# Kernel optimization log

Measured on AMD Instinct MI355X. Metric: run time of the kernel, lower is better.

The kernel has to match this reference:

```python
import jax, jax.numpy as jnp
import numpy as np

R = 64      # residual_channels
S = 128     # skip_channels
N_BLOCKS = 3
N_LAYERS = 10
L = N_BLOCKS * N_LAYERS  # 30 dilated blocks total


def _causal_conv_k2(x, W, b, dilation):
    """Causal dilated conv1d with kernel_size=2.
    x: [B, Cin, T], W: [Cout, Cin, 2], b: [Cout].
    out[t] = W[:,:,0] @ x[t - dilation] + W[:,:,1] @ x[t] + b  (zero-padded).
    """
    x_prev = jnp.pad(x, ((0, 0), (0, 0), (dilation, 0)))[:, :, :-dilation]
    return (jnp.einsum('oc,bct->bot', W[:, :, 0], x_prev)
            + jnp.einsum('oc,bct->bot', W[:, :, 1], x)
            + b[None, :, None])


def _conv1x1(x, W, b):
    # W: [Cout, Cin, 1]
    return jnp.einsum('oc,bct->bot', W[:, :, 0], x) + b[None, :, None]


def setup_inputs() -> dict:
    key = jax.random.key(0)
    ks = jax.random.split(key, 16)
    sc = 0.1
    inp = {
        'x': jax.random.normal(ks[0], (4, 1, 16384), dtype=jnp.float32),
        'w_causal': jax.random.normal(ks[1], (R, 1, 2), dtype=jnp.float32) * sc,
        'b_causal': jnp.zeros((R,), dtype=jnp.float32),
        'Wf': jax.random.normal(ks[2], (L, R, R, 2), dtype=jnp.float32) * sc,
        'bf': jnp.zeros((L, R), dtype=jnp.float32),
        'Wg': jax.random.normal(ks[3], (L, R, R, 2), dtype=jnp.float32) * sc,
        'bg': jnp.zeros((L, R), dtype=jnp.float32),
        'Wr': jax.random.normal(ks[4], (L, R, R, 1), dtype=jnp.float32) * sc,
        'br': jnp.zeros((L, R), dtype=jnp.float32),
        'Ws': jax.random.normal(ks[5], (L, S, R, 1), dtype=jnp.float32) * sc,
        'bs': jnp.zeros((L, S), dtype=jnp.float32),
        'w_post': jax.random.normal(ks[6], (S, S, 1), dtype=jnp.float32) * sc,
        'b_post': jnp.zeros((S,), dtype=jnp.float32),
        'w_o1': jax.random.normal(ks[7], (S, S, 1), dtype=jnp.float32) * sc,
        'b_o1': jnp.zeros((S,), dtype=jnp.float32),
        'w_o2': jax.random.normal(ks[8], (1, S, 1), dtype=jnp.float32) * sc,
        'b_o2': jnp.zeros((1,), dtype=jnp.float32),
    }
    return inp


def reference(x, w_causal, b_causal, Wf, bf, Wg, bg, Wr, br, Ws, bs,
              w_post, b_post, w_o1, b_o1, w_o2, b_o2):
    # initial causal conv (kernel 2, dilation 1): [B,1,T] -> [B,R,T]
    h = _causal_conv_k2(x, w_causal, b_causal, 1)
    skip_sum = jnp.zeros((h.shape[0], S, h.shape[2]), dtype=h.dtype)
    for i in range(L):
        d = 2 ** (i % N_LAYERS)
        f = jnp.tanh(_causal_conv_k2(h, Wf[i], bf[i], d))
        g = jax.nn.sigmoid(_causal_conv_k2(h, Wg[i], bg[i], d))
        out = f * g
        h = _conv1x1(out, Wr[i], br[i]) + h
        skip_sum = skip_sum + _conv1x1(out, Ws[i], bs[i])
    s = jax.nn.relu(_conv1x1(skip_sum, w_post, b_post))
    s = jax.nn.relu(_conv1x1(s, w_o1, b_o1))
    return _conv1x1(s, w_o2, b_o2)  # [B, 1, T]
```

## Files before the change

kernel.cpp:

```cpp
#include <hip/hip_runtime.h>

#define RCH 64
#define SCH 128
#define NLAYERS 30
#define TLEN 16384
#define NB 4
#define LSTR 72

typedef _Float16 f16;
typedef _Float16 f16x8 __attribute__((ext_vector_type(8)));
typedef float f32x4 __attribute__((ext_vector_type(4)));

__global__ __launch_bounds__(256) void pack_all(
    const float* __restrict__ Wf, const float* __restrict__ Wg,
    const float* __restrict__ Wr, const float* __restrict__ Ws,
    const float* __restrict__ w_post, const float* __restrict__ w_o1,
    f16* __restrict__ wfgp, f16* __restrict__ wrsp,
    f16* __restrict__ wpostp, f16* __restrict__ wo1pp)
{
    int id = blockIdx.x * 256 + threadIdx.x;
    const int N1 = NLAYERS * 8 * 4 * 64;
    const int N2 = NLAYERS * 12 * 2 * 64;
    const int N3 = 8 * 4 * 64;
    union { f16 h8[8]; uint4 u; } pk;
    if (id < N1) {
        int l = id & 63, kt = (id >> 6) & 3, mt = (id >> 8) & 7, i = id >> 11;
        int m = mt * 16 + (l & 15);
        int kb = kt * 32 + (l >> 4) * 8;
        #pragma unroll
        for (int j = 0; j < 8; ++j) {
            int k = kb + j, tap = k >> 6, c = k & 63;
            float v = (m < 64) ? Wf[(((i * 64 + m) * 64 + c) << 1) + tap]
                               : Wg[(((i * 64 + m - 64) * 64 + c) << 1) + tap];
            pk.h8[j] = (f16)v;
        }
        *(uint4*)&wfgp[(size_t)id * 8] = pk.u;
    } else if (id < N1 + N2) {
        int id2 = id - N1;
        int l = id2 & 63, kt = (id2 >> 6) & 1, mt = (id2 >> 7) % 12, i = id2 / 1536;
        int m = mt * 16 + (l & 15);
        int cb = kt * 32 + (l >> 4) * 8;
        #pragma unroll
        for (int j = 0; j < 8; ++j) {
            int c = cb + j;
            float v = (m < 64) ? Wr[(i * 64 + m) * 64 + c]
                               : Ws[(i * 128 + m - 64) * 64 + c];
            pk.h8[j] = (f16)v;
        }
        *(uint4*)&wrsp[(size_t)id2 * 8] = pk.u;
    } else if (id < N1 + N2 + 2 * N3) {
        int id3 = id - N1 - N2;
        const float* src = (id3 < N3) ? w_post : w_o1;
        f16* dst = (id3 < N3) ? wpostp : wo1pp;
        int id4 = id3 & (N3 - 1);
        int l = id4 & 63, kt = (id4 >> 6) & 3, mt = (id4 >> 8) & 7;
        int m = mt * 16 + (l & 15);
        int cb = kt * 32 + (l >> 4) * 8;
        #pragma unroll
        for (int j = 0; j < 8; ++j)
            pk.h8[j] = (f16)src[m * 128 + cb + j];
        *(uint4*)&dst[(size_t)id4 * 8] = pk.u;
    }
}

__global__ __launch_bounds__(256) void init_f16(
    const float* __restrict__ x, const float* __restrict__ wc,
    const float* __restrict__ bc, f16* __restrict__ h)
{
    int id = blockIdx.x * 256 + threadIdx.x;
    int t = id & (TLEN - 1);
    float xc = x[id];
    float xp = (t > 0) ? x[id - 1] : 0.f;
    f16* dst = h + (size_t)id * 64;
    #pragma unroll
    for (int c0 = 0; c0 < 64; c0 += 8) {
        union { f16 h8[8]; uint4 u; } pk;
        #pragma unroll
        for (int j = 0; j < 8; ++j) {
            int c = c0 + j;
            pk.h8[j] = (f16)fmaf(wc[2 * c], xp, fmaf(wc[2 * c + 1], xc, bc[c]));
        }
        *(uint4*)&dst[c0] = pk.u;
    }
}

__global__ __launch_bounds__(256, 4) void layer_mfma(
    const f16* __restrict__ hin, f16* __restrict__ hout, f16* __restrict__ skipw,
    const f16* __restrict__ wfgp, const f16* __restrict__ wrsp,
    const float* __restrict__ bf, const float* __restrict__ bg,
    const float* __restrict__ br, const float* __restrict__ bs,
    int layer, int dil, int first)
{
    __shared__ f16 hcurT[64 * LSTR];
    __shared__ f16 hprvT[64 * LSTR];
    __shared__ f16 outT [64 * LSTR];
    int tid = threadIdx.x, lane = tid & 63, wv = tid >> 6;
    int kg = lane >> 4, ln = lane & 15;
    int bx = blockIdx.x, b = bx >> 8, t0 = (bx & 255) * 64;
    const f16* hb = hin + (size_t)b * TLEN * 64;

    {
        int row = tid >> 2, q = tid & 3;
        const f16* src = hb + (size_t)(t0 + row) * 64;
        *(uint4*)&hcurT[row * LSTR + q * 8]       = *(const uint4*)&src[q * 8];
        *(uint4*)&hcurT[row * LSTR + (q + 4) * 8] = *(const uint4*)&src[(q + 4) * 8];
        int tp = t0 + row - dil;
        if (tp >= 0) {
            const f16* sp = hb + (size_t)tp * 64;
            *(uint4*)&hprvT[row * LSTR + q * 8]       = *(const uint4*)&sp[q * 8];
            *(uint4*)&hprvT[row * LSTR + (q + 4) * 8] = *(const uint4*)&sp[(q + 4) * 8];
        } else {
            uint4 z = make_uint4(0, 0, 0, 0);
            *(uint4*)&hprvT[row * LSTR + q * 8]       = z;
            *(uint4*)&hprvT[row * LSTR + (q + 4) * 8] = z;
        }
    }
    __syncthreads();

    const f16* wl = wfgp + (size_t)layer * 32 * 64 * 8;
    f16x8 a0[4], a1[4];
    #pragma unroll
    for (int kt = 0; kt < 4; ++kt) {
        a0[kt] = *(const f16x8*)&wl[(size_t)((wv * 4 + kt) * 64 + lane) * 8];
        a1[kt] = *(const f16x8*)&wl[(size_t)(((wv + 4) * 4 + kt) * 64 + lane) * 8];
    }
    f32x4 af[4], ag[4];
    {
        float4 bvf = *(const float4*)(bf + layer * 64 + wv * 16 + kg * 4);
        float4 bvg = *(const float4*)(bg + layer * 64 + wv * 16 + kg * 4);
        #pragma unroll
        for (int ts = 0; ts < 4; ++ts) {
            af[ts] = (f32x4){bvf.x, bvf.y, bvf.z, bvf.w};
            ag[ts] = (f32x4){bvg.x, bvg.y, bvg.z, bvg.w};
        }
    }
    #pragma unroll
    for (int ts = 0; ts < 4; ++ts) {
        #pragma unroll
        for (int kt = 0; kt < 4; ++kt) {
            const f16* tile = (kt < 2) ? hprvT : hcurT;
            f16x8 bb = *(const f16x8*)&tile[(ts * 16 + ln) * LSTR + (kt & 1) * 32 + kg * 8];
            af[ts] = __builtin_amdgcn_mfma_f32_16x16x32_f16(a0[kt], bb, af[ts], 0, 0, 0);
            ag[ts] = __builtin_amdgcn_mfma_f32_16x16x32_f16(a1[kt], bb, ag[ts], 0, 0, 0);
        }
    }

    #pragma unroll
    for (int ts = 0; ts < 4; ++ts) {
        union { f16 h[4]; uint2 u; } pk;
        #pragma unroll
        for (int r = 0; r < 4; ++r) {
            float fv = af[ts][r], gv = ag[ts][r];
            float e2 = __expf(2.f * fv);
            float th = 1.f - 2.f * __builtin_amdgcn_rcpf(e2 + 1.f);
            float sg = __builtin_amdgcn_rcpf(1.f + __expf(-gv));
            pk.h[r] = (f16)(th * sg);
        }
        *(uint2*)&outT[(ts * 16 + ln) * LSTR + wv * 16 + kg * 4] = pk.u;
    }
    __syncthreads();

    const f16* wl2 = wrsp + (size_t)layer * 24 * 64 * 8;
    int mt0 = wv * 3;
    f16x8 a2[3][2];
    #pragma unroll
    for (int m = 0; m < 3; ++m)
        #pragma unroll
        for (int kt = 0; kt < 2; ++kt)
            a2[m][kt] = *(const f16x8*)&wl2[(size_t)(((mt0 + m) * 2 + kt) * 64 + lane) * 8];
    f32x4 ac[3][4];
    #pragma unroll
    for (int m = 0; m < 3; ++m) {
        int mtt = mt0 + m;
        const float* bp = (mtt < 4) ? (br + layer * 64 + mtt * 16 + kg * 4)
                                    : (bs + layer * 128 + (mtt - 4) * 16 + kg * 4);
        float4 bv = *(const float4*)bp;
        #pragma unroll
        for (int ts = 0; ts < 4; ++ts)
            ac[m][ts] = (f32x4){bv.x, bv.y, bv.z, bv.w};
    }
    #pragma unroll
    for (int ts = 0; ts < 4; ++ts) {
        #pragma unroll
        for (int kt = 0; kt < 2; ++kt) {
            f16x8 bb = *(const f16x8*)&outT[(ts * 16 + ln) * LSTR + kt * 32 + kg * 8];
            #pragma unroll
            for (int m = 0; m < 3; ++m)
                ac[m][ts] = __builtin_amdgcn_mfma_f32_16x16x32_f16(a2[m][kt], bb, ac[m][ts], 0, 0, 0);
        }
    }

    f16* sb = skipw + (size_t)b * TLEN * 128;
    #pragma unroll
    for (int m = 0; m < 3; ++m) {
        int mtt = mt0 + m;
        if (mtt < 4) {
            int o = mtt * 16 + kg * 4;
            #pragma unroll
            for (int ts = 0; ts < 4; ++ts) {
                int t = ts * 16 + ln;
                union { f16 h[4]; uint2 u; } ho, hn;
                ho.u = *(const uint2*)&hcurT[t * LSTR + o];
                #pragma unroll
                for (int r = 0; r < 4; ++r)
                    hn.h[r] = (f16)(ac[m][ts][r] + (float)ho.h[r]);
                *(uint2*)&hout[((size_t)b * TLEN + t0 + t) * 64 + o] = hn.u;
            }
        } else {
            int oc = (mtt - 4) * 16 + kg * 4;
            #pragma unroll
            for (int ts = 0; ts < 4; ++ts) {
                int t = ts * 16 + ln;
                union { f16 h[4]; uint2 u; } sv;
                if (first) {
                    #pragma unroll
                    for (int r = 0; r < 4; ++r) sv.h[r] = (f16)ac[m][ts][r];
                } else {
                    union { f16 h[4]; uint2 u; } old;
                    old.u = *(const uint2*)&sb[(size_t)(t0 + t) * 128 + oc];
                    #pragma unroll
                    for (int r = 0; r < 4; ++r)
                        sv.h[r] = (f16)(ac[m][ts][r] + (float)old.h[r]);
                }
                *(uint2*)&sb[(size_t)(t0 + t) * 128 + oc] = sv.u;
            }
        }
    }
}

__global__ __launch_bounds__(256, 4) void head_mfma(
    const f16* __restrict__ skipw, const f16* __restrict__ wpostp,
    const f16* __restrict__ wo1pp, const float* __restrict__ wo2,
    const float* __restrict__ b_post, const float* __restrict__ b_o1,
    const float* __restrict__ b_o2, float* __restrict__ out)
{
    __shared__ f16 sT[64 * 136];
    int tid = threadIdx.x, lane = tid & 63, wv = tid >> 6;
    int kg = lane >> 4, ln = lane & 15;
    int bx = blockIdx.x, b = bx >> 8, t0 = (bx & 255) * 64;
    int trow = wv * 16 + ln;
    int tl = t0 + trow;
    const f16* sb = skipw + (size_t)b * TLEN * 128;

    f16x8 bfr[4];
    #pragma unroll
    for (int kt = 0; kt < 4; ++kt)
        bfr[kt] = *(const f16x8*)&sb[(size_t)tl * 128 + kt * 32 + kg * 8];
    f32x4 acc[8];
    #pragma unroll
    for (int mt = 0; mt < 8; ++mt) {
        float4 bv = *(const float4*)(b_post + mt * 16 + kg * 4);
        acc[mt] = (f32x4){bv.x, bv.y, bv.z, bv.w};
    }
    #pragma unroll
    for (int mt = 0; mt < 8; ++mt)
        #pragma unroll
        for (int kt = 0; kt < 4; ++kt) {
            f16x8 a = *(const f16x8*)&wpostp[(size_t)((mt * 4 + kt) * 64 + lane) * 8];
            acc[mt] = __builtin_amdgcn_mfma_f32_16x16x32_f16(a, bfr[kt], acc[mt], 0, 0, 0);
        }
    #pragma unroll
    for (int mt = 0; mt < 8; ++mt) {
        union { f16 h[4]; uint2 u; } pk;
        #pragma unroll
        for (int r = 0; r < 4; ++r)
            pk.h[r] = (f16)fmaxf(acc[mt][r], 0.f);
        *(uint2*)&sT[trow * 136 + mt * 16 + kg * 4] = pk.u;
    }

    f16x8 b2[4];
    #pragma unroll
    for (int kt = 0; kt < 4; ++kt)
        b2[kt] = *(const f16x8*)&sT[trow * 136 + kt * 32 + kg * 8];
    f32x4 acc2[8];
    #pragma unroll
    for (int mt = 0; mt < 8; ++mt) {
        float4 bv = *(const float4*)(b_o1 + mt * 16 + kg * 4);
        acc2[mt] = (f32x4){bv.x, bv.y, bv.z, bv.w};
    }
    #pragma unroll
    for (int mt = 0; mt < 8; ++mt)
        #pragma unroll
        for (int kt = 0; kt < 4; ++kt) {
            f16x8 a = *(const f16x8*)&wo1pp[(size_t)((mt * 4 + kt) * 64 + lane) * 8];
            acc2[mt] = __builtin_amdgcn_mfma_f32_16x16x32_f16(a, b2[kt], acc2[mt], 0, 0, 0);
        }

    float part = 0.f;
    #pragma unroll
    for (int mt = 0; mt < 8; ++mt) {
        float4 wv4 = *(const float4*)(wo2 + mt * 16 + kg * 4);
        part = fmaf(wv4.x, fmaxf(acc2[mt][0], 0.f), part);
        part = fmaf(wv4.y, fmaxf(acc2[mt][1], 0.f), part);
        part = fmaf(wv4.z, fmaxf(acc2[mt][2], 0.f), part);
        part = fmaf(wv4.w, fmaxf(acc2[mt][3], 0.f), part);
    }
    part += __shfl_xor(part, 16);
    part += __shfl_xor(part, 32);
    if (lane < 16)
        out[(size_t)b * TLEN + tl] = part + b_o2[0];
}

extern "C" void kernel_launch(void* const* d_in, const int* in_sizes, int n_in,
                              void* d_out, int out_size, void* d_ws, size_t ws_size,
                              hipStream_t stream) {
    const float* x        = (const float*)d_in[0];
    const float* w_causal = (const float*)d_in[1];
    const float* b_causal = (const float*)d_in[2];
    const float* Wf       = (const float*)d_in[3];
    const float* bf       = (const float*)d_in[4];
    const float* Wg       = (const float*)d_in[5];
    const float* bg       = (const float*)d_in[6];
    const float* Wr       = (const float*)d_in[7];
    const float* br       = (const float*)d_in[8];
    const float* Ws       = (const float*)d_in[9];
    const float* bs       = (const float*)d_in[10];
    const float* w_post   = (const float*)d_in[11];
    const float* b_post   = (const float*)d_in[12];
    const float* w_o1     = (const float*)d_in[13];
    const float* b_o1     = (const float*)d_in[14];
    const float* w_o2     = (const float*)d_in[15];
    const float* b_o2     = (const float*)d_in[16];

    f16* p     = (f16*)d_ws;
    f16* h0    = p;  p += (size_t)NB * TLEN * 64;
    f16* h1    = p;  p += (size_t)NB * TLEN * 64;
    f16* skipw = p;  p += (size_t)NB * TLEN * 128;
    f16* wfgp  = p;  p += (size_t)NLAYERS * 8 * 4 * 64 * 8;
    f16* wrsp  = p;  p += (size_t)NLAYERS * 12 * 2 * 64 * 8;
    f16* wpostp= p;  p += (size_t)8 * 4 * 64 * 8;
    f16* wo1pp = p;

    pack_all<<<436, 256, 0, stream>>>(Wf, Wg, Wr, Ws, w_post, w_o1,
                                      wfgp, wrsp, wpostp, wo1pp);
    init_f16<<<NB * TLEN / 256, 256, 0, stream>>>(x, w_causal, b_causal, h0);

    f16* hin = h0;
    f16* hout = h1;
    for (int i = 0; i < NLAYERS; ++i) {
        int d = 1 << (i % 10);
        layer_mfma<<<1024, 256, 0, stream>>>(hin, hout, skipw, wfgp, wrsp,
                                             bf, bg, br, bs, i, d, i == 0);
        f16* tmp = hin; hin = hout; hout = tmp;
    }
    head_mfma<<<1024, 256, 0, stream>>>(skipw, wpostp, wo1pp, w_o2,
                                        b_post, b_o1, b_o2, (float*)d_out);
}
```

Baseline: 672.7 us.

## Stage layer outputs through LDS for coalesced writes and prefetch skip accumulator

The new residual h and skip contributions are first written into shared-memory tiles, then copied out to global memory with coalesced 16-byte row stores, replacing the scattered 8-byte stores. The previous skip-sum values are loaded at kernel start, so their global latency overlaps the MFMA work. This adds a fourth LDS buffer, extra barriers and 16 live registers for the prefetched skip data, which may lower occupancy.

```diff
diff --git a/kernel.cpp b/kernel.cpp
--- a/kernel.cpp
+++ b/kernel.cpp
@@ -94,13 +94,23 @@
     __shared__ f16 hcurT[64 * LSTR];
     __shared__ f16 hprvT[64 * LSTR];
     __shared__ f16 outT [64 * LSTR];
+    __shared__ f16 extT [64 * LSTR];
     int tid = threadIdx.x, lane = tid & 63, wv = tid >> 6;
     int kg = lane >> 4, ln = lane & 15;
     int bx = blockIdx.x, b = bx >> 8, t0 = (bx & 255) * 64;
     const f16* hb = hin + (size_t)b * TLEN * 64;
+    f16* sb = skipw + (size_t)b * TLEN * 128;
+    int row = tid >> 2, q = tid & 3;
+
+    uint4 sold[4];
+    if (!first) {
+        const f16* srow = sb + (size_t)(t0 + row) * 128 + q * 32;
+        #pragma unroll
+        for (int k = 0; k < 4; ++k)
+            sold[k] = *(const uint4*)&srow[k * 8];
+    }
 
     {
-        int row = tid >> 2, q = tid & 3;
         const f16* src = hb + (size_t)(t0 + row) * 64;
         *(uint4*)&hcurT[row * LSTR + q * 8]       = *(const uint4*)&src[q * 8];
         *(uint4*)&hcurT[row * LSTR + (q + 4) * 8] = *(const uint4*)&src[(q + 4) * 8];
@@ -158,7 +168,6 @@
         }
         *(uint2*)&outT[(ts * 16 + ln) * LSTR + wv * 16 + kg * 4] = pk.u;
     }
-    __syncthreads();
 
     const f16* wl2 = wrsp + (size_t)layer * 24 * 64 * 8;
     int mt0 = wv * 3;
@@ -168,6 +177,8 @@
         #pragma unroll
         for (int kt = 0; kt < 2; ++kt)
             a2[m][kt] = *(const f16x8*)&wl2[(size_t)(((mt0 + m) * 2 + kt) * 64 + lane) * 8];
+    __syncthreads();
+
     f32x4 ac[3][4];
     #pragma unroll
     for (int m = 0; m < 3; ++m) {
@@ -189,8 +200,8 @@
                 ac[m][ts] = __builtin_amdgcn_mfma_f32_16x16x32_f16(a2[m][kt], bb, ac[m][ts], 0, 0, 0);
         }
     }
-
-    f16* sb = skipw + (size_t)b * TLEN * 128;
+    __syncthreads();
+
     #pragma unroll
     for (int m = 0; m < 3; ++m) {
         int mtt = mt0 + m;
@@ -204,25 +215,45 @@
                 #pragma unroll
                 for (int r = 0; r < 4; ++r)
                     hn.h[r] = (f16)(ac[m][ts][r] + (float)ho.h[r]);
-                *(uint2*)&hout[((size_t)b * TLEN + t0 + t) * 64 + o] = hn.u;
+                *(uint2*)&hprvT[t * LSTR + o] = hn.u;
             }
         } else {
-            int oc = (mtt - 4) * 16 + kg * 4;
+            f16* dstT = (mtt < 8) ? outT : extT;
+            int ch = ((mtt - 4) & 3) * 16 + kg * 4;
             #pragma unroll
             for (int ts = 0; ts < 4; ++ts) {
                 int t = ts * 16 + ln;
                 union { f16 h[4]; uint2 u; } sv;
-                if (first) {
-                    #pragma unroll
-                    for (int r = 0; r < 4; ++r) sv.h[r] = (f16)ac[m][ts][r];
-                } else {
-                    union { f16 h[4]; uint2 u; } old;
-                    old.u = *(const uint2*)&sb[(size_t)(t0 + t) * 128 + oc];
-                    #pragma unroll
-                    for (int r = 0; r < 4; ++r)
-                        sv.h[r] = (f16)(ac[m][ts][r] + (float)old.h[r]);
-                }
-                *(uint2*)&sb[(size_t)(t0 + t) * 128 + oc] = sv.u;
+                #pragma unroll
+                for (int r = 0; r < 4; ++r) sv.h[r] = (f16)ac[m][ts][r];
+                *(uint2*)&dstT[t * LSTR + ch] = sv.u;
+            }
+        }
+    }
+    __syncthreads();
+
+    {
+        f16* hrow = hout + ((size_t)b * TLEN + t0 + row) * 64 + q * 16;
+        *(uint4*)&hrow[0] = *(const uint4*)&hprvT[row * LSTR + q * 16];
+        *(uint4*)&hrow[8] = *(const uint4*)&hprvT[row * LSTR + q * 16 + 8];
+    }
+    {
+        f16* drow = sb + (size_t)(t0 + row) * 128 + q * 32;
+        const f16* incb = ((q < 2) ? outT : extT) + row * LSTR + (q & 1) * 32;
+        if (first) {
+            #pragma unroll
+            for (int k = 0; k < 4; ++k)
+                *(uint4*)&drow[k * 8] = *(const uint4*)&incb[k * 8];
+        } else {
+            #pragma unroll
+            for (int k = 0; k < 4; ++k) {
+                union { f16 h[8]; uint4 u; } o_, i_, n_;
+                o_.u = sold[k];
+                i_.u = *(const uint4*)&incb[k * 8];
+                #pragma unroll
+                for (int j = 0; j < 8; ++j)
+                    n_.h[j] = (f16)((float)o_.h[j] + (float)i_.h[j]);
+                *(uint4*)&drow[k * 8] = n_.u;
             }
         }
     }
```

Result: faster. 645.5 us (-4.1%).
